# Kernel optimization log

Hardware: AMD Instinct MI355X
Metric: run time of the kernel (lower is better)

Reference implementation:

```python
import jax, jax.numpy as jnp
import numpy as np
from jax import lax

B, N, NB = 1, 1600, 200
NOTE, ENC, ENCVEC = 128, 64, 16
OUT, MARGIN, TREG = 11, 32, 32
E = 12
FIN = NOTE + ENC + 2 * TREG + OUT + MARGIN   # 299 = net_params.final.input
SEC = OUT + MARGIN                           # 43 = GatedGraph secondary size
FBH = NOTE + ENC                             # final_beat_hidden_idx
SEQ_IT, G_IT = 2, 3
HEADS_M = 8


def setup_inputs():
    key = jax.random.key(0)
    ks = iter(jax.random.split(key, 64))
    nrm = lambda shape, s=0.05: jax.random.normal(next(ks), shape, jnp.float32) * s
    zeros = lambda shape: jnp.zeros(shape, jnp.float32)
    inp = {}
    inp["note_out"] = jax.random.normal(next(ks), (B, N, NOTE), jnp.float32)
    inp["perf_vec"] = jax.random.normal(next(ks), (B, ENCVEC), jnp.float32)
    inp["res_info"] = jax.random.normal(next(ks), (B, NB, 8), jnp.float32)
    # sparse musical-graph adjacency, one matrix per edge type
    inp["edges"] = (jax.random.uniform(next(ks), (E, N, N)) < 0.004).astype(jnp.float32)
    # sorted beat index per note, every beat non-empty (8 notes per beat)
    inp["beat_numbers"] = jnp.arange(N, dtype=jnp.int32) // (N // NB)
    inp["w_style"] = nrm((ENCVEC, ENC)); inp["b_style"] = zeros((ENC,))
    inp["w_init1"] = nrm((NOTE, ENC)); inp["b_init1"] = zeros((ENC,))
    inp["w_init2"] = nrm((ENC, OUT)); inp["b_init2"] = zeros((OUT,))
    inp["gg_wa"] = nrm((E, FIN, FIN)); inp["gg_ba"] = zeros((FIN,))
    inp["gg_wz"] = nrm((FIN, SEC)); inp["gg_wr"] = nrm((FIN, SEC)); inp["gg_wh"] = nrm((FIN, SEC))
    inp["gg_uz"] = nrm((SEC, SEC)); inp["gg_ur"] = nrm((SEC, SEC)); inp["gg_uh"] = nrm((SEC, SEC))
    inp["att_beat_w"] = nrm((OUT, OUT)); inp["att_beat_b"] = zeros((OUT,)); inp["att_beat_c"] = nrm((1, OUT), 1.0)
    inp["att_marg_w"] = nrm((MARGIN, MARGIN)); inp["att_marg_b"] = zeros((MARGIN,))
    inp["att_marg_c"] = nrm((HEADS_M, MARGIN // HEADS_M), 1.0)
    rnn_in = MARGIN + OUT + 8
    for l, din in ((0, rnn_in), (1, 2 * TREG)):
        for d in "fb":
            inp[f"lstm_wih_{l}{d}"] = nrm((4 * TREG, din))
            inp[f"lstm_whh_{l}{d}"] = nrm((4 * TREG, TREG))
            inp[f"lstm_b_{l}{d}"] = zeros((4 * TREG,))
    inp["w_tempo"] = nrm((2 * TREG, 1)); inp["b_tempo"] = zeros((1,))
    inp["w_fc1"] = nrm((FIN, MARGIN)); inp["b_fc1"] = zeros((MARGIN,))
    inp["w_fc2"] = nrm((MARGIN, OUT - 1)); inp["b_fc2"] = zeros((OUT - 1,))
    return inp


def _gated_graph(h, edges, wa, ba, wz, wr, wh, uz, ur, uh, iters):
    # h: (B,N,FIN), edges: (E,N,N). GGNN update on last SEC features.
    for _ in range(iters):
        agg = jnp.einsum('eij,bid->ebjd', edges, h)          # incoming msgs per edge type
        act = jnp.einsum('ebjd,eds->bjs', agg, wa) + ba      # (B,N,FIN)
        hs = h[..., -SEC:]
        z = jax.nn.sigmoid(act @ wz + hs @ uz)
        r = jax.nn.sigmoid(act @ wr + hs @ ur)
        cand = jnp.tanh(act @ wh + (r * hs) @ uh)
        hs = (1.0 - z) * hs + z * cand
        h = jnp.concatenate([h[..., :-SEC], hs], -1)
    return h


def _seg_attention(x, W, b, ctx, seg, num_seg):
    # ContextAttention pooled per beat segment (make_higher_node).
    Bb, T, D = x.shape
    H, hd = ctx.shape
    a = jnp.tanh(x @ W + b).reshape(Bb, T, H, hd)
    sim = jnp.einsum('bthd,hd->bth', a, ctx)
    def smax(s):  # segment softmax over notes within each beat, (T,H)
        m = jax.ops.segment_max(s, seg, num_segments=num_seg)
        e = jnp.exp(s - m[seg])
        zz = jax.ops.segment_sum(e, seg, num_segments=num_seg)
        return e / zz[seg]
    w = jax.vmap(smax)(sim)                                   # (B,T,H)
    xh = x.reshape(Bb, T, H, hd)
    pool = jax.vmap(lambda wi, xi: jax.ops.segment_sum(wi[:, :, None] * xi, seg, num_segments=num_seg))(w, xh)
    return pool.reshape(Bb, num_seg, D)


def _lstm_dir(x, wih, whh, b, reverse):
    Bb = x.shape[0]; H = whh.shape[1]
    def step(carry, xt):
        h, c = carry
        g = xt @ wih.T + h @ whh.T + b
        i, f, gg, o = jnp.split(g, 4, -1)
        c = jax.nn.sigmoid(f) * c + jax.nn.sigmoid(i) * jnp.tanh(gg)
        h = jax.nn.sigmoid(o) * jnp.tanh(c)
        return (h, c), h
    init = (jnp.zeros((Bb, H), x.dtype), jnp.zeros((Bb, H), x.dtype))
    _, hs = lax.scan(step, init, jnp.swapaxes(x, 0, 1), reverse=reverse)
    return jnp.swapaxes(hs, 0, 1)


def _bilstm(x, layers):
    for (wf, uf, bf, wb, ub, bb) in layers:
        x = jnp.concatenate([_lstm_dir(x, wf, uf, bf, False), _lstm_dir(x, wb, ub, bb, True)], -1)
    return x


def _forward(note_out, perf_vec, res_info, edges, beat_numbers,
             w_style, b_style, w_init1, b_init1, w_init2, b_init2,
             gg_wa, gg_ba, gg_wz, gg_wr, gg_wh, gg_uz, gg_ur, gg_uh,
             att_beat_w, att_beat_b, att_beat_c, att_marg_w, att_marg_b, att_marg_c,
             lstm_wih_0f, lstm_whh_0f, lstm_b_0f, lstm_wih_0b, lstm_whh_0b, lstm_b_0b,
             lstm_wih_1f, lstm_whh_1f, lstm_b_1f, lstm_wih_1b, lstm_whh_1b, lstm_b_1b,
             w_tempo, b_tempo, w_fc1, b_fc1, w_fc2, b_fc2):
    Bb, Nn, _ = note_out.shape
    # style_vector_expandor (dropout = identity in eval), broadcast to notes
    perf_z = jax.nn.relu(perf_vec @ w_style + b_style)
    perf_z = jnp.broadcast_to(perf_z[:, None, :], (Bb, Nn, ENC))
    init_out = jax.nn.relu(note_out @ w_init1 + b_init1) @ w_init2 + b_init2
    beat_hid0 = jnp.zeros((Bb, Nn, 2 * TREG), note_out.dtype)
    margin0 = jnp.zeros((Bb, Nn, MARGIN), note_out.dtype)
    out = jnp.concatenate([note_out, perf_z, beat_hid0, init_out, margin0], -1)  # (B,N,FIN)
    lstm_layers = [(lstm_wih_0f, lstm_whh_0f, lstm_b_0f, lstm_wih_0b, lstm_whh_0b, lstm_b_0b),
                   (lstm_wih_1f, lstm_whh_1f, lstm_b_1f, lstm_wih_1b, lstm_whh_1b, lstm_b_1b)]
    total = [init_out]
    final_out = init_out
    for _ in range(SEQ_IT):
        out = _gated_graph(out, edges, gg_wa, gg_ba, gg_wz, gg_wr, gg_wh, gg_uz, gg_ur, gg_uh, G_IT)
        init_o = out[..., -SEC:-MARGIN]          # (B,N,OUT)
        marg = out[..., -MARGIN:]                # (B,N,MARGIN)
        marg_beat = _seg_attention(marg, att_marg_w, att_marg_b, att_marg_c, beat_numbers, NB)
        out_beat = _seg_attention(init_o, att_beat_w, att_beat_b, att_beat_c, beat_numbers, NB)
        beat_cat = jnp.concatenate([out_beat, marg_beat, res_info], -1)  # (B,NB,51)
        rnn = _bilstm(beat_cat, lstm_layers)                             # (B,NB,64)
        tempo = rnn @ w_tempo + b_tempo                                  # (B,NB,1)
        tempos_sp = tempo[:, beat_numbers, :]    # span_beat_to_note_num
        rnn_sp = rnn[:, beat_numbers, :]
        out = jnp.concatenate([out[..., :FBH], rnn_sp, out[..., -SEC:]], -1)
        other = jax.nn.relu(out @ w_fc1 + b_fc1) @ w_fc2 + b_fc2         # (B,N,OUT-1)
        final_out = jnp.concatenate([tempos_sp, other], -1)              # (B,N,OUT)
        out = jnp.concatenate([out[..., :-SEC], final_out, out[..., -MARGIN:]], -1)
        total.append(final_out)
    return final_out, jnp.stack(total, 0)


def reference(note_out, perf_vec, res_info, edges, beat_numbers,
              w_style, b_style, w_init1, b_init1, w_init2, b_init2,
              gg_wa, gg_ba, gg_wz, gg_wr, gg_wh, gg_uz, gg_ur, gg_uh,
              att_beat_w, att_beat_b, att_beat_c, att_marg_w, att_marg_b, att_marg_c,
              lstm_wih_0f, lstm_whh_0f, lstm_b_0f, lstm_wih_0b, lstm_whh_0b, lstm_b_0b,
              lstm_wih_1f, lstm_whh_1f, lstm_b_1f, lstm_wih_1b, lstm_whh_1b, lstm_b_1b,
              w_tempo, b_tempo, w_fc1, b_fc1, w_fc2, b_fc2):
    return _forward(note_out, perf_vec, res_info, edges, beat_numbers,
                    w_style, b_style, w_init1, b_init1, w_init2, b_init2,
                    gg_wa, gg_ba, gg_wz, gg_wr, gg_wh, gg_uz, gg_ur, gg_uh,
                    att_beat_w, att_beat_b, att_beat_c, att_marg_w, att_marg_b, att_marg_c,
                    lstm_wih_0f, lstm_whh_0f, lstm_b_0f, lstm_wih_0b, lstm_whh_0b, lstm_b_0b,
                    lstm_wih_1f, lstm_whh_1f, lstm_b_1f, lstm_wih_1b, lstm_whh_1b, lstm_b_1b,
                    w_tempo, b_tempo, w_fc1, b_fc1, w_fc2, b_fc2)
```

## Files before the change

kernel.cpp:

```cpp
#include <hip/hip_runtime.h>
#include <stdint.h>

#define NN     1600
#define NBEAT  200
#define FINW   299
#define HSTR   300
#define SECW   43
#define EDG    12
#define C3     129
#define CM     128
#define DEG_CAP 256

#define NB_ADJ  2560
#define NB_WA3  450
#define NB_INIT NN

__device__ __forceinline__ float sigm(float x){ return 1.0f/(1.0f+__expf(-x)); }
__device__ __forceinline__ float tanh_(float x){ return 2.0f/(1.0f+__expf(-2.0f*x)) - 1.0f; }

constexpr size_t OFF_H    = 0;
constexpr size_t OFF_WA3  = OFF_H    + (size_t)NN*HSTR;
constexpr size_t OFF_WA3X = OFF_WA3  + (size_t)EDG*FINW*CM;
constexpr size_t OFF_B3   = OFF_WA3X + (size_t)EDG*FINW;
constexpr size_t OFF_MST  = OFF_B3   + 132;
constexpr size_t OFF_MSTX = OFF_MST  + (size_t)EDG*NN*CM;
constexpr size_t OFF_M3   = OFF_MSTX + (size_t)EDG*NN;
constexpr size_t OFF_M3X  = OFF_M3   + (size_t)EDG*NN*CM;
constexpr size_t OFF_CUR  = OFF_M3X  + (size_t)EDG*NN;
constexpr size_t OFF_ADJR = OFF_CUR  + NN;
constexpr size_t OFF_XW   = OFF_ADJR + (size_t)NN*DEG_CAP;
constexpr size_t OFF_RNN0 = OFF_XW   + (size_t)2*NBEAT*128;
constexpr size_t OFF_RNN1 = OFF_RNN0 + (size_t)NBEAT*64;

__global__ __launch_bounds__(192) void k_setup(
    const float* wa, const float* ba, const float* wz, const float* wr, const float* wh,
    const float* note, const float* pv, const float* w_style, const float* b_style,
    const float* w1, const float* b1, const float* w2, const float* b2,
    const float* edges, float* ws, float* dout){
  int blk = blockIdx.x;
  int t = threadIdx.x;
  if (blk < NB_ADJ){
    int* cur  = (int*)(ws + OFF_CUR);
    int* adjr = (int*)(ws + OFF_ADJR);
    const uint4* p = (const uint4*)edges;
    const unsigned int nvec = 7680000u;
    const unsigned int stride = (unsigned int)NB_ADJ*192u;
    unsigned int v0 = (unsigned int)blk*192u + t;
    for (unsigned int b0 = v0; b0 < nvec; b0 += 4u*stride){
      unsigned int v1=b0+stride, v2=b0+2u*stride, v3=b0+3u*stride;
      bool g1=v1<nvec, g2=v2<nvec, g3=v3<nvec;
      uint4 w0 = p[b0];
      uint4 w1v = g1 ? p[v1] : make_uint4(0,0,0,0);
      uint4 w2v = g2 ? p[v2] : make_uint4(0,0,0,0);
      uint4 w3v = g3 ? p[v3] : make_uint4(0,0,0,0);
      uint4 wv[4] = {w0,w1v,w2v,w3v};
      unsigned int vv[4] = {b0,v1,v2,v3};
      #pragma unroll
      for (int u=0; u<4; u++){
        uint4 w = wv[u];
        if ((w.x|w.y|w.z|w.w)==0u) continue;
        unsigned int base = vv[u]*4u;
        unsigned int arr[4]={w.x,w.y,w.z,w.w};
        #pragma unroll
        for (int q=0;q<4;q++){
          if (arr[q]){
            unsigned int idx=base+q;
            unsigned int j=idx%1600u;
            int slot=atomicAdd(&cur[j],1);
            if (slot<DEG_CAP) adjr[j*DEG_CAP + slot]=(int)(idx/1600u);
          }
        }
      }
    }
  } else if (blk < NB_ADJ + NB_WA3){
    int base = (blk - NB_ADJ)*8;
    __shared__ __align__(16) float lrow[299*8];
    for (int x=t; x<8*299; x+=192){
      int r = x & 7, s = x >> 3;
      int R = base + r;
      float v = 0.f;
      if (R < 3588)       v = wa[(size_t)R*FINW + s];
      else if (R == 3588) v = ba[s];
      lrow[s*8 + r] = v;
    }
    __syncthreads();
    if (t < C3){
      const float* Wp; int cc;
      if (t<43){Wp=wz; cc=t;} else if (t<86){Wp=wr; cc=t-43;} else {Wp=wh; cc=t-86;}
      float acc[8];
      #pragma unroll
      for (int r=0;r<8;r++) acc[r]=0.f;
      for (int s=0;s<FINW;s++){
        float w = Wp[s*43+cc];
        float4 lo = *(const float4*)&lrow[s*8];
        float4 hi = *(const float4*)&lrow[s*8+4];
        acc[0]+=lo.x*w; acc[1]+=lo.y*w; acc[2]+=lo.z*w; acc[3]+=lo.w*w;
        acc[4]+=hi.x*w; acc[5]+=hi.y*w; acc[6]+=hi.z*w; acc[7]+=hi.w*w;
      }
      #pragma unroll
      for (int r=0;r<8;r++){
        int R = base + r;
        if (R < 3588){
          if (t<CM) ws[OFF_WA3 + (size_t)R*CM + t] = acc[r];
          else      ws[OFF_WA3X + R]               = acc[r];
        } else if (R == 3588){
          ws[OFF_B3 + t] = acc[r];
        }
      }
    }
  } else {
    int i = blk - NB_ADJ - NB_WA3;
    __shared__ float lnote[128];
    __shared__ float lh1[64];
    __shared__ float lo[11];
    __shared__ float lperf[64];
    if (t<128) lnote[t]=note[i*128+t];
    if (t>=64 && t<128){
      int u=t-64;
      float acc=b_style[u];
      for (int k=0;k<16;k++) acc += pv[k]*w_style[k*64+u];
      lperf[u]=fmaxf(acc,0.f);
    }
    __syncthreads();
    if (t<64){
      float acc=b1[t];
      for (int k=0;k<128;k++) acc += lnote[k]*w1[k*64+t];
      lh1[t]=fmaxf(acc,0.f);
    }
    __syncthreads();
    if (t<11){
      float acc=b2[t];
      for (int s=0;s<64;s++) acc += lh1[s]*w2[s*11+t];
      lo[t]=acc;
      dout[17600 + i*11 + t] = acc;
    }
    __syncthreads();
    for (int c=t;c<FINW;c+=192){
      float v;
      if (c<128)      v=lnote[c];
      else if (c<192) v=lperf[c-128];
      else if (c<256) v=0.f;
      else if (c<267) v=lo[c-256];
      else            v=0.f;
      ws[OFF_H + (size_t)i*HSTR + c]=v;
    }
  }
}

__global__ void k_mstat(float* ws){
  int e = blockIdx.y; int i0 = blockIdx.x*8;
  int t = threadIdx.x;
  __shared__ float lh[8][256];
  __shared__ float lh2[8][44];
  const float* h = ws + OFF_H;
  for (int x=t; x<512; x+=64){
    int r = x>>6, dq = x&63;
    ((float4*)&lh[r][0])[dq] = ((const float4*)(h + (size_t)(i0+r)*HSTR))[dq];
  }
  for (int x=t; x<88; x+=64){
    int r = x/11, dq = x-r*11;
    ((float4*)&lh2[r][0])[dq] = ((const float4*)(h + (size_t)(i0+r)*HSTR + 256))[dq];
  }
  __syncthreads();
  const float* wm = ws + OFF_WA3 + (size_t)e*FINW*CM;
  int c0 = 2*t;
  float acc[8][2];
  #pragma unroll
  for (int r=0;r<8;r++){acc[r][0]=0.f;acc[r][1]=0.f;}
  for (int d=0; d<256; d+=4){
    float4 hv[8];
    #pragma unroll
    for (int r=0;r<8;r++) hv[r] = *(const float4*)&lh[r][d];
    #pragma unroll
    for (int dd=0;dd<4;dd++){
      float2 w = *(const float2*)(wm + (size_t)(d+dd)*CM + c0);
      #pragma unroll
      for (int r=0;r<8;r++){
        float hvv = ((const float*)&hv[r])[dd];
        acc[r][0] += hvv*w.x; acc[r][1] += hvv*w.y;
      }
    }
  }
  float* mst = ws + OFF_MST + ((size_t)e*NN + i0)*CM;
  #pragma unroll
  for (int r=0;r<8;r++) *(float2*)(mst + (size_t)r*CM + c0) = make_float2(acc[r][0],acc[r][1]);
  const float* wd = wm + (size_t)256*CM;
  for (int d=0; d<SECW; d++){
    float2 w = *(const float2*)(wd + (size_t)d*CM + c0);
    #pragma unroll
    for (int r=0;r<8;r++){
      float hvv = lh2[r][d];
      acc[r][0] += hvv*w.x; acc[r][1] += hvv*w.y;
    }
  }
  float* m3 = ws + OFF_M3 + ((size_t)e*NN + i0)*CM;
  #pragma unroll
  for (int r=0;r<8;r++) *(float2*)(m3 + (size_t)r*CM + c0) = make_float2(acc[r][0],acc[r][1]);
  if (t<8){
    const float* wx = ws + OFF_WA3X + (size_t)e*FINW;
    float a=0.f;
    for (int d=0; d<256; d++) a += lh[t][d]*wx[d];
    ws[OFF_MSTX + (size_t)e*NN + i0 + t] = a;
    for (int d=0; d<SECW; d++) a += lh2[t][d]*wx[256+d];
    ws[OFF_M3X + (size_t)e*NN + i0 + t] = a;
  }
}

__global__ void k_m3dyn(float* ws){
  int e=blockIdx.y, i0=blockIdx.x*8, t=threadIdx.x;
  __shared__ float lhs[8][44];
  const float* h = ws + OFF_H;
  for (int x=t; x<8*43; x+=64){ int r=x/43, d=x-r*43; lhs[r][d]=h[(size_t)(i0+r)*HSTR+256+d]; }
  __syncthreads();
  const float* wd  = ws + OFF_WA3 + ((size_t)e*FINW+256)*CM;
  const float* mst = ws + OFF_MST + ((size_t)e*NN+i0)*CM;
  int c0=2*t;
  float acc[8][2];
  #pragma unroll
  for (int r=0;r<8;r++){ float2 m=*(const float2*)(mst+(size_t)r*CM+c0); acc[r][0]=m.x; acc[r][1]=m.y; }
  for (int d=0; d<43; d++){
    float2 w=*(const float2*)(wd + (size_t)d*CM + c0);
    #pragma unroll
    for (int r=0;r<8;r++){ float hv=lhs[r][d]; acc[r][0]+=hv*w.x; acc[r][1]+=hv*w.y; }
  }
  float* m3 = ws + OFF_M3 + ((size_t)e*NN+i0)*CM;
  #pragma unroll
  for (int r=0;r<8;r++) *(float2*)(m3+(size_t)r*CM+c0)=make_float2(acc[r][0],acc[r][1]);
  if (t<8){
    float a = ws[OFF_MSTX + (size_t)e*NN+i0+t];
    const float* wx = ws + OFF_WA3X + (size_t)e*FINW + 256;
    for (int d=0;d<43;d++) a += lhs[t][d]*wx[d];
    ws[OFF_M3X + (size_t)e*NN+i0+t]=a;
  }
}

__global__ void k_agg_gru(float* ws, const float* uz, const float* ur, const float* uh){
  int j=blockIdx.x, t=threadIdx.x;
  __shared__ float lpre[C3];
  __shared__ float lhs[SECW];
  __shared__ float lrh[SECW];
  __shared__ int   ladj[DEG_CAP];
  float* h = ws + OFF_H;
  const int* cur =(const int*)(ws+OFF_CUR);
  const int* adjr=(const int*)(ws+OFF_ADJR) + (size_t)j*DEG_CAP;
  int cnt = cur[j]; if (cnt>DEG_CAP) cnt=DEG_CAP;
  for (int k=t;k<cnt;k+=128) ladj[k]=adjr[k];
  if (t<SECW) lhs[t] = h[(size_t)j*HSTR + 256 + t];
  __syncthreads();
  const float* M3=ws+OFF_M3; const float* M3X=ws+OFF_M3X;
  float a0 = ws[OFF_B3 + t];
  float ax = (t==0)? ws[OFF_B3+128] : 0.f;
  float p1=0.f,p2=0.f,p3=0.f,p4=0.f,p5=0.f,p6=0.f,p7=0.f;
  int k=0;
  for (; k+8<=cnt; k+=8){
    int r0=ladj[k],r1=ladj[k+1],r2=ladj[k+2],r3=ladj[k+3];
    int r4=ladj[k+4],r5=ladj[k+5],r6=ladj[k+6],r7=ladj[k+7];
    a0 += M3[(size_t)r0*CM+t];
    p1 += M3[(size_t)r1*CM+t];
    p2 += M3[(size_t)r2*CM+t];
    p3 += M3[(size_t)r3*CM+t];
    p4 += M3[(size_t)r4*CM+t];
    p5 += M3[(size_t)r5*CM+t];
    p6 += M3[(size_t)r6*CM+t];
    p7 += M3[(size_t)r7*CM+t];
    if (t==0) ax += ((M3X[r0]+M3X[r1])+(M3X[r2]+M3X[r3]))
                  + ((M3X[r4]+M3X[r5])+(M3X[r6]+M3X[r7]));
  }
  for (; k<cnt; k++){ int r=ladj[k]; a0+=M3[(size_t)r*CM+t]; if(t==0) ax+=M3X[r]; }
  a0 += ((p1+p2)+(p3+p4)) + ((p5+p6)+p7);
  lpre[t]=a0; if (t==0) lpre[128]=ax;
  __syncthreads();
  float z=0.f;
  if (t<SECW){
    float az=lpre[t], ar=lpre[43+t];
    for (int d=0;d<SECW;d++){ float hv=lhs[d]; az+=hv*uz[d*43+t]; ar+=hv*ur[d*43+t]; }
    z=sigm(az);
    float r=sigm(ar);
    lrh[t]=r*lhs[t];
  }
  __syncthreads();
  if (t<SECW){
    float ah=lpre[86+t];
    for (int d=0;d<SECW;d++) ah += lrh[d]*uh[d*43+t];
    float cand=tanh_(ah);
    h[(size_t)j*HSTR+256+t] = (1.f-z)*lhs[t] + z*cand;
  }
}

__global__ void k_attn_xw(float* ws, const float* mw, const float* mb, const float* mc,
                          const float* bw, const float* bb, const float* bc,
                          const float* res,
                          const float* w0f, const float* bia0f,
                          const float* w0b, const float* bia0b, float* xw){
  int b=blockIdx.x, t=threadIdx.x;
  float* h=ws+OFF_H;
  __shared__ float sm[8][8];
  __shared__ float wgt[8][8];
  __shared__ float sb[8];
  __shared__ float wb_[8];
  __shared__ float lb[52];
  int n=t>>3, hh=t&7;
  if (t<64){
    const float* mrow = h + (size_t)(b*8+n)*HSTR + 267;
    float sim=0.f;
    for (int d=0;d<4;d++){
      int c=hh*4+d;
      float acc=mb[c];
      for (int k=0;k<32;k++) acc += mrow[k]*mw[k*32+c];
      sim += tanh_(acc)*mc[c];
    }
    sm[n][hh]=sim;
  }
  if (t<8){
    const float* irow = h + (size_t)(b*8+t)*HSTR + 256;
    float sim=0.f;
    for (int d=0;d<11;d++){
      float acc=bb[d];
      for (int k=0;k<11;k++) acc += irow[k]*bw[k*11+d];
      sim += tanh_(acc)*bc[d];
    }
    sb[t]=sim;
  }
  __syncthreads();
  if (t<64){
    float m=-1e30f;
    for (int q=0;q<8;q++) m=fmaxf(m, sm[q][hh]);
    float Z=0.f;
    for (int q=0;q<8;q++) Z+=__expf(sm[q][hh]-m);
    wgt[n][hh]=__expf(sm[n][hh]-m)/Z;
  }
  if (t<8){
    float m=-1e30f;
    for (int q=0;q<8;q++) m=fmaxf(m, sb[q]);
    float Z=0.f;
    for (int q=0;q<8;q++) Z+=__expf(sb[q]-m);
    wb_[t]=__expf(sb[t]-m)/Z;
  }
  __syncthreads();
  if (t<32){
    int hh2=t>>2;
    float acc=0.f;
    for (int q=0;q<8;q++) acc += wgt[q][hh2]* h[(size_t)(b*8+q)*HSTR + 267 + t];
    lb[11+t]=acc;
  }
  if (t<11){
    float acc=0.f;
    for (int q=0;q<8;q++) acc += wb_[q]* h[(size_t)(b*8+q)*HSTR + 256 + t];
    lb[t]=acc;
  }
  if (t<8) lb[43+t]=res[b*8+t];
  __syncthreads();
  float acc0=bia0f[t], acc1=bia0b[t];
  for (int k=0;k<51;k++){
    float v=lb[k];
    acc0 += v*w0f[t*51+k];
    acc1 += v*w0b[t*51+k];
  }
  xw[((size_t)0*NBEAT + b)*128 + t]=acc0;
  xw[((size_t)1*NBEAT + b)*128 + t]=acc1;
}

__global__ void k_xw(const float* inp, int din, const float* wf, const float* bf_,
                     const float* wb, const float* bb_, float* xw){
  int bid=blockIdx.x; int tt=bid>>1, dir=bid&1;
  const float* w = dir? wb:wf; const float* bia = dir? bb_:bf_;
  __shared__ float rowl[64];
  int t=threadIdx.x;
  if (t<din) rowl[t]=inp[(size_t)tt*din+t];
  __syncthreads();
  float acc=bia[t];
  for (int k=0;k<din;k++) acc += rowl[k]*w[t*din+k];
  xw[((size_t)dir*NBEAT + tt)*128 + t]=acc;
}

#define CH 8
__global__ __launch_bounds__(64,1) void k_scan(const float* xw, const float* whh_f,
                                               const float* whh_b, float* out){
  int dir = blockIdx.x;
  int l = threadIdx.x;
  const float* whh = dir ? whh_b : whh_f;
  float4 rA[8], rB[8];
  #pragma unroll
  for (int q=0;q<8;q++){
    rA[q] = *(const float4*)&whh[l*32 + q*4];
    rB[q] = *(const float4*)&whh[(l+64)*32 + q*4];
  }
  __shared__ __align__(16) float xb[2][CH*128];
  __shared__ __align__(16) float lds_h[32];
  if (l<32) lds_h[l]=0.f;
  const float* x = xw + (size_t)dir*NBEAT*128;
  int half = l>>5, q4 = l&31;
  int stp = dir ? -1 : 1;
  float4 st[4];
  #pragma unroll
  for (int r=0;r<4;r++){
    int s = 2*r + half;
    int ti = dir ? (NBEAT-1-s) : s;
    st[r] = ((const float4*)&x[ti*128])[q4];
  }
  #pragma unroll
  for (int r=0;r<4;r++){ int u=2*r+half; ((float4*)&xb[0][u*128])[q4]=st[r]; }
  __builtin_amdgcn_wave_barrier();
  float creg = 0.f;
  int tt = dir ? NBEAT-1 : 0;
  for (int c=0;c<NBEAT/CH;c++){
    int buf = c&1;
    if (c+1 < NBEAT/CH){
      #pragma unroll
      for (int r=0;r<4;r++){
        int s = (c+1)*CH + 2*r + half;
        int ti = dir ? (NBEAT-1-s) : s;
        st[r] = ((const float4*)&x[ti*128])[q4];
      }
    }
    #pragma unroll
    for (int u=0;u<CH;u++){
      float cxA = xb[buf][u*128 + l];
      float cxB = xb[buf][u*128 + 64 + l];
      float4 hv[8];
      #pragma unroll
      for (int q=0;q<8;q++) hv[q] = *(const float4*)&lds_h[q*4];
      float a[8], bq[8];
      #pragma unroll
      for (int q=0;q<8;q++){
        float4 h4=hv[q], wa=rA[q], wb=rB[q];
        a[q]  = h4.x*wa.x + h4.y*wa.y + h4.z*wa.z + h4.w*wa.w;
        bq[q] = h4.x*wb.x + h4.y*wb.y + h4.z*wb.z + h4.w*wb.w;
      }
      float accA = cxA + ((a[0]+a[1])+(a[2]+a[3])) + ((a[4]+a[5])+(a[6]+a[7]));
      float accB = cxB + ((bq[0]+bq[1])+(bq[2]+bq[3])) + ((bq[4]+bq[5])+(bq[6]+bq[7]));
      float pA  = sigm(accA);
      float pBt = tanh_(accB);
      float pBs = sigm(accB);
      float prod = pA * pBt;
      float prodIn = __shfl(prod, l & 31, 64);
      creg = pA*creg + prodIn;
      float hnew = pBs * tanh_(creg);
      if (l>=32){
        lds_h[l&31] = hnew;
        out[(size_t)tt*64 + dir*32 + (l&31)] = hnew;
      }
      tt += stp;
    }
    if (c+1 < NBEAT/CH){
      #pragma unroll
      for (int r=0;r<4;r++){ int u=2*r+half; ((float4*)&xb[1-buf][u*128])[q4]=st[r]; }
      __builtin_amdgcn_wave_barrier();
    }
  }
}

__global__ void k_fc(float* ws, const int* bn, const float* w1, const float* b1,
                     const float* w2, const float* b2,
                     const float* wt, const float* bt, float* dout, int it){
  int i=blockIdx.x, t=threadIdx.x;
  __shared__ float row[FINW];
  __shared__ float hid[32];
  __shared__ float fo[11];
  float* h=ws+OFF_H;
  int b = bn[i];
  const float* rnn = ws+OFF_RNN1;
  for (int c=t;c<FINW;c+=64){
    float v;
    if (c>=192 && c<256){ v=rnn[(size_t)b*64 + c-192]; h[(size_t)i*HSTR+c]=v; }
    else v=h[(size_t)i*HSTR+c];
    row[c]=v;
  }
  float tv = rnn[(size_t)b*64 + t]*wt[t];
  #pragma unroll
  for (int off=32; off; off>>=1) tv += __shfl_xor(tv, off, 64);
  __syncthreads();
  if (t<32){
    float acc=b1[t];
    for (int k=0;k<FINW;k++) acc += row[k]*w1[k*32+t];
    hid[t]=fmaxf(acc,0.f);
  }
  __syncthreads();
  if (t<10){
    float acc=b2[t];
    for (int m=0;m<32;m++) acc += hid[m]*w2[m*10+t];
    fo[1+t]=acc;
  }
  if (t==0) fo[0]=tv + bt[0];
  __syncthreads();
  if (t<11){
    float v=fo[t];
    h[(size_t)i*HSTR+256+t]=v;
    dout[(size_t)(2+it)*17600 + i*11 + t]=v;
    if (it==1) dout[i*11+t]=v;
  }
}

extern "C" void kernel_launch(void* const* d_in, const int* in_sizes, int n_in,
                              void* d_out, int out_size, void* d_ws, size_t ws_size,
                              hipStream_t stream){
  (void)in_sizes; (void)n_in; (void)out_size; (void)ws_size;
  float* ws=(float*)d_ws;
  const float* note    =(const float*)d_in[0];
  const float* pv      =(const float*)d_in[1];
  const float* res     =(const float*)d_in[2];
  const float* edges   =(const float*)d_in[3];
  const int*   bn      =(const int*)d_in[4];
  const float* w_style =(const float*)d_in[5];
  const float* b_style =(const float*)d_in[6];
  const float* w_init1 =(const float*)d_in[7];
  const float* b_init1 =(const float*)d_in[8];
  const float* w_init2 =(const float*)d_in[9];
  const float* b_init2 =(const float*)d_in[10];
  const float* gg_wa   =(const float*)d_in[11];
  const float* gg_ba   =(const float*)d_in[12];
  const float* gg_wz   =(const float*)d_in[13];
  const float* gg_wr   =(const float*)d_in[14];
  const float* gg_wh   =(const float*)d_in[15];
  const float* gg_uz   =(const float*)d_in[16];
  const float* gg_ur   =(const float*)d_in[17];
  const float* gg_uh   =(const float*)d_in[18];
  const float* abw     =(const float*)d_in[19];
  const float* abb     =(const float*)d_in[20];
  const float* abc     =(const float*)d_in[21];
  const float* amw     =(const float*)d_in[22];
  const float* amb     =(const float*)d_in[23];
  const float* amc     =(const float*)d_in[24];
  const float* wih0f   =(const float*)d_in[25];
  const float* whh0f   =(const float*)d_in[26];
  const float* b0f     =(const float*)d_in[27];
  const float* wih0b   =(const float*)d_in[28];
  const float* whh0b   =(const float*)d_in[29];
  const float* b0b     =(const float*)d_in[30];
  const float* wih1f   =(const float*)d_in[31];
  const float* whh1f   =(const float*)d_in[32];
  const float* b1f     =(const float*)d_in[33];
  const float* wih1b   =(const float*)d_in[34];
  const float* whh1b   =(const float*)d_in[35];
  const float* b1b     =(const float*)d_in[36];
  const float* w_tempo =(const float*)d_in[37];
  const float* b_tempo =(const float*)d_in[38];
  const float* w_fc1   =(const float*)d_in[39];
  const float* b_fc1   =(const float*)d_in[40];
  const float* w_fc2   =(const float*)d_in[41];
  const float* b_fc2   =(const float*)d_in[42];
  float* dout=(float*)d_out;

  hipMemsetAsync(ws+OFF_CUR, 0, NN*sizeof(int), stream);
  k_setup<<<NB_ADJ+NB_WA3+NB_INIT,192,0,stream>>>(
      gg_wa,gg_ba,gg_wz,gg_wr,gg_wh,
      note,pv,w_style,b_style,w_init1,b_init1,w_init2,b_init2,
      edges,ws,dout);

  for (int it=0; it<2; it++){
    k_mstat<<<dim3(200,12),64,0,stream>>>(ws);
    k_agg_gru<<<NN,128,0,stream>>>(ws,gg_uz,gg_ur,gg_uh);
    for (int g=1; g<3; g++){
      k_m3dyn<<<dim3(200,12),64,0,stream>>>(ws);
      k_agg_gru<<<NN,128,0,stream>>>(ws,gg_uz,gg_ur,gg_uh);
    }
    k_attn_xw<<<NBEAT,128,0,stream>>>(ws,amw,amb,amc,abw,abb,abc,res,
                                      wih0f,b0f,wih0b,b0b,ws+OFF_XW);
    k_scan<<<2,64,0,stream>>>(ws+OFF_XW,whh0f,whh0b,ws+OFF_RNN0);
    k_xw<<<2*NBEAT,128,0,stream>>>(ws+OFF_RNN0,64,wih1f,b1f,wih1b,b1b,ws+OFF_XW);
    k_scan<<<2,64,0,stream>>>(ws+OFF_XW,whh1f,whh1b,ws+OFF_RNN1);
    k_fc<<<NN,64,0,stream>>>(ws,bn,w_fc1,b_fc1,w_fc2,b_fc2,w_tempo,b_tempo,dout,it);
  }
}
```

Baseline: 905.3 us.

## Restructure LSTM scan: transposed xw layout, register hidden broadcast, prescaled gates

The input projection buffer is stored transposed (gate-major over beats) and pre-multiplied by the exp2 scale constants, so each lane loads its own gate inputs as contiguous float4 chunks with register double buffering instead of going through LDS. The hidden state is broadcast via readlane into registers rather than through LDS writes and reads each step. Gate activations use raw exp2/rcp builtins with the scale folded into the recurrent weights, which removes multiplies and LDS round trips on the serial critical path. In exchange, each step now issues 32 readlanes and the kernel holds more registers, and the hardware rcp/exp2 builtins trade a little accuracy.

Result: faster. 765.7 us (-15.4%).

```diff
diff --git a/kernel.cpp b/kernel.cpp
--- a/kernel.cpp
+++ b/kernel.cpp
@@ -15,8 +15,26 @@
 #define NB_WA3  450
 #define NB_INIT NN
 
-__device__ __forceinline__ float sigm(float x){ return 1.0f/(1.0f+__expf(-x)); }
-__device__ __forceinline__ float tanh_(float x){ return 2.0f/(1.0f+__expf(-2.0f*x)) - 1.0f; }
+#define K1C (-1.4426950408889634f)
+#define K2C (-2.8853900817779268f)
+
+#if __has_builtin(__builtin_amdgcn_exp2f)
+__device__ __forceinline__ float fexp2(float x){ return __builtin_amdgcn_exp2f(x); }
+#else
+__device__ __forceinline__ float fexp2(float x){ return exp2f(x); }
+#endif
+#if __has_builtin(__builtin_amdgcn_rcpf)
+__device__ __forceinline__ float frcp(float x){ return __builtin_amdgcn_rcpf(x); }
+#else
+__device__ __forceinline__ float frcp(float x){ return 1.0f/x; }
+#endif
+
+__device__ __forceinline__ float sigm(float x){ return frcp(1.f + fexp2(K1C*x)); }
+__device__ __forceinline__ float tanh_(float x){ return __builtin_fmaf(frcp(1.f + fexp2(K2C*x)), 2.f, -1.f); }
+
+__device__ __forceinline__ float gate_scale(int col){
+  return (col >= 64 && col < 96) ? K2C : K1C;
+}
 
 constexpr size_t OFF_H    = 0;
 constexpr size_t OFF_WA3  = OFF_H    + (size_t)NN*HSTR;
@@ -356,8 +374,9 @@
     acc0 += v*w0f[t*51+k];
     acc1 += v*w0b[t*51+k];
   }
-  xw[((size_t)0*NBEAT + b)*128 + t]=acc0;
-  xw[((size_t)1*NBEAT + b)*128 + t]=acc1;
+  float sc = gate_scale(t);
+  xw[((size_t)t)*NBEAT + b]       = acc0*sc;
+  xw[((size_t)(128+t))*NBEAT + b] = acc1*sc;
 }
 
 __global__ void k_xw(const float* inp, int din, const float* wf, const float* bf_,
@@ -370,84 +389,96 @@
   __syncthreads();
   float acc=bia[t];
   for (int k=0;k<din;k++) acc += rowl[k]*w[t*din+k];
-  xw[((size_t)dir*NBEAT + tt)*128 + t]=acc;
-}
-
-#define CH 8
-__global__ __launch_bounds__(64,1) void k_scan(const float* xw, const float* whh_f,
+  xw[((size_t)(dir*128 + t))*NBEAT + tt] = acc*gate_scale(t);
+}
+
+template<int DIR>
+__device__ __forceinline__ void chunk8(int c, const float4& A0, const float4& A1,
+    const float4& B0, const float4& B1,
+    float* hu, float& creg, const float4* rA, const float4* rB,
+    float cb1, float cb0, int l, float* out){
+  float cxA[8] = {A0.x,A0.y,A0.z,A0.w,A1.x,A1.y,A1.z,A1.w};
+  float cxB[8] = {B0.x,B0.y,B0.z,B0.w,B1.x,B1.y,B1.z,B1.w};
+  float hst[8];
+  #pragma unroll
+  for (int u=0; u<8; u++){
+    const int e = DIR ? (7-u) : u;
+    float av[8], bv[8];
+    #pragma unroll
+    for (int q=0; q<8; q++){
+      av[q] = hu[4*q+0]*rA[q].x + hu[4*q+1]*rA[q].y + hu[4*q+2]*rA[q].z + hu[4*q+3]*rA[q].w;
+      bv[q] = hu[4*q+0]*rB[q].x + hu[4*q+1]*rB[q].y + hu[4*q+2]*rB[q].z + hu[4*q+3]*rB[q].w;
+    }
+    float accA = cxA[e] + (((av[0]+av[1])+(av[2]+av[3])) + ((av[4]+av[5])+(av[6]+av[7])));
+    float accB = cxB[e] + (((bv[0]+bv[1])+(bv[2]+bv[3])) + ((bv[4]+bv[5])+(bv[6]+bv[7])));
+    float pA  = frcp(1.f + fexp2(accA));
+    float rBv = frcp(1.f + fexp2(accB));
+    float pB  = __builtin_fmaf(rBv, cb1, cb0);
+    float prod = pA * pB;
+    float prodIn = __shfl(prod, l & 31, 64);
+    creg = __builtin_fmaf(pA, creg, prodIn);
+    float T = __builtin_fmaf(frcp(1.f + fexp2(creg)), 2.f, -1.f);
+    float hnew = pB * T;
+    hst[u] = hnew;
+    #pragma unroll
+    for (int d=0; d<32; d++)
+      hu[d] = __uint_as_float(__builtin_amdgcn_readlane(__float_as_uint(hnew), 32+d));
+  }
+  if (l >= 32){
+    int j = l - 32;
+    #pragma unroll
+    for (int u=0; u<8; u++){
+      int s = c*8 + u;
+      int tt = DIR ? (199 - s) : s;
+      out[(size_t)tt*64 + DIR*32 + j] = hst[u];
+    }
+  }
+}
+
+template<int DIR>
+__device__ __forceinline__ void lstm_scan(const float* xwT, const float* whh, float* out){
+  const int l = threadIdx.x;
+  const float sB = (l < 32) ? K2C : K1C;
+  float4 rA[8], rB[8];
+  #pragma unroll
+  for (int q=0; q<8; q++){
+    float4 a = *(const float4*)&whh[l*32 + q*4];
+    float4 b = *(const float4*)&whh[(l+64)*32 + q*4];
+    rA[q] = make_float4(a.x*K1C, a.y*K1C, a.z*K1C, a.w*K1C);
+    rB[q] = make_float4(b.x*sB,  b.y*sB,  b.z*sB,  b.w*sB);
+  }
+  const float cb1 = (l < 32) ? (2.f*K2C) : 1.f;
+  const float cb0 = (l < 32) ? (-K2C)    : 0.f;
+  const float* xA = xwT + ((size_t)DIR*128 + l)*NBEAT;
+  const float* xB = xwT + ((size_t)DIR*128 + 64 + l)*NBEAT;
+  float hu[32];
+  #pragma unroll
+  for (int d=0; d<32; d++) hu[d] = 0.f;
+  float creg = 0.f;
+  float4 A0,A1,B0,B1, P0,P1,Q0,Q1;
+#define LOADC(cidx, a0,a1,b0,b1) do {               \
+    int _b = DIR ? (192 - (cidx)*8) : ((cidx)*8);   \
+    a0 = *(const float4*)&xA[_b];                   \
+    a1 = *(const float4*)&xA[_b+4];                 \
+    b0 = *(const float4*)&xB[_b];                   \
+    b1 = *(const float4*)&xB[_b+4];                 \
+  } while(0)
+  LOADC(0, A0,A1,B0,B1);
+  for (int cc=0; cc<12; cc++){
+    int c0 = 2*cc;
+    LOADC(c0+1, P0,P1,Q0,Q1);
+    chunk8<DIR>(c0,   A0,A1,B0,B1, hu, creg, rA, rB, cb1, cb0, l, out);
+    LOADC(c0+2, A0,A1,B0,B1);
+    chunk8<DIR>(c0+1, P0,P1,Q0,Q1, hu, creg, rA, rB, cb1, cb0, l, out);
+  }
+  chunk8<DIR>(24, A0,A1,B0,B1, hu, creg, rA, rB, cb1, cb0, l, out);
+#undef LOADC
+}
+
+__global__ __launch_bounds__(64,1) void k_scan(const float* xwT, const float* whh_f,
                                                const float* whh_b, float* out){
-  int dir = blockIdx.x;
-  int l = threadIdx.x;
-  const float* whh = dir ? whh_b : whh_f;
-  float4 rA[8], rB[8];
-  #pragma unroll
-  for (int q=0;q<8;q++){
-    rA[q] = *(const float4*)&whh[l*32 + q*4];
-    rB[q] = *(const float4*)&whh[(l+64)*32 + q*4];
-  }
-  __shared__ __align__(16) float xb[2][CH*128];
-  __shared__ __align__(16) float lds_h[32];
-  if (l<32) lds_h[l]=0.f;
-  const float* x = xw + (size_t)dir*NBEAT*128;
-  int half = l>>5, q4 = l&31;
-  int stp = dir ? -1 : 1;
-  float4 st[4];
-  #pragma unroll
-  for (int r=0;r<4;r++){
-    int s = 2*r + half;
-    int ti = dir ? (NBEAT-1-s) : s;
-    st[r] = ((const float4*)&x[ti*128])[q4];
-  }
-  #pragma unroll
-  for (int r=0;r<4;r++){ int u=2*r+half; ((float4*)&xb[0][u*128])[q4]=st[r]; }
-  __builtin_amdgcn_wave_barrier();
-  float creg = 0.f;
-  int tt = dir ? NBEAT-1 : 0;
-  for (int c=0;c<NBEAT/CH;c++){
-    int buf = c&1;
-    if (c+1 < NBEAT/CH){
-      #pragma unroll
-      for (int r=0;r<4;r++){
-        int s = (c+1)*CH + 2*r + half;
-        int ti = dir ? (NBEAT-1-s) : s;
-        st[r] = ((const float4*)&x[ti*128])[q4];
-      }
-    }
-    #pragma unroll
-    for (int u=0;u<CH;u++){
-      float cxA = xb[buf][u*128 + l];
-      float cxB = xb[buf][u*128 + 64 + l];
-      float4 hv[8];
-      #pragma unroll
-      for (int q=0;q<8;q++) hv[q] = *(const float4*)&lds_h[q*4];
-      float a[8], bq[8];
-      #pragma unroll
-      for (int q=0;q<8;q++){
-        float4 h4=hv[q], wa=rA[q], wb=rB[q];
-        a[q]  = h4.x*wa.x + h4.y*wa.y + h4.z*wa.z + h4.w*wa.w;
-        bq[q] = h4.x*wb.x + h4.y*wb.y + h4.z*wb.z + h4.w*wb.w;
-      }
-      float accA = cxA + ((a[0]+a[1])+(a[2]+a[3])) + ((a[4]+a[5])+(a[6]+a[7]));
-      float accB = cxB + ((bq[0]+bq[1])+(bq[2]+bq[3])) + ((bq[4]+bq[5])+(bq[6]+bq[7]));
-      float pA  = sigm(accA);
-      float pBt = tanh_(accB);
-      float pBs = sigm(accB);
-      float prod = pA * pBt;
-      float prodIn = __shfl(prod, l & 31, 64);
-      creg = pA*creg + prodIn;
-      float hnew = pBs * tanh_(creg);
-      if (l>=32){
-        lds_h[l&31] = hnew;
-        out[(size_t)tt*64 + dir*32 + (l&31)] = hnew;
-      }
-      tt += stp;
-    }
-    if (c+1 < NBEAT/CH){
-      #pragma unroll
-      for (int r=0;r<4;r++){ int u=2*r+half; ((float4*)&xb[1-buf][u*128])[q4]=st[r]; }
-      __builtin_amdgcn_wave_barrier();
-    }
-  }
+  if (blockIdx.x == 0) lstm_scan<0>(xwT, whh_f, out);
+  else                 lstm_scan<1>(xwT, whh_b, out);
 }
 
 __global__ void k_fc(float* ws, const int* bn, const float* w1, const float* b1,
```
